# Performance work log

Measured on AMD Instinct MI355X. Metric: run time of the kernel, lower is better.

The kernel has to match this reference:

```python
import jax, jax.numpy as jnp
import numpy as np

VOCAB, EMBED, PROJ = 200000, 300, 128
B, S = 16, 2048


def setup_inputs() -> dict:
    key = jax.random.key(0)
    k1, k2, k3, k4, k5 = jax.random.split(key, 5)
    ext_word_ids = jax.random.randint(k1, (B, S), 0, VOCAB)
    seq_lengths = jax.random.randint(k2, (B,), 1, S + 1)  # at least 1 token per sentence
    embed = jax.random.normal(k3, (VOCAB, EMBED), dtype=jnp.float32)
    embed = embed.at[0].set(0.0)  # padding_idx = 0 row is zero
    W = jax.random.normal(k4, (PROJ, EMBED), dtype=jnp.float32) * 0.05
    b = jax.random.normal(k5, (PROJ,), dtype=jnp.float32) * 0.05
    return {"ext_word_ids": ext_word_ids, "seq_lengths": seq_lengths,
            "embed": embed, "W": W, "b": b}


def reference(ext_word_ids, seq_lengths, embed, W, b):
    # Dedup in the original is purely an optimization; math is:
    # out[b, t] = W @ embed[ids[b, t]] + b  for t < seq_lengths[b], else 0.
    x = embed[ext_word_ids]                       # [B, S, E] gather
    y = jnp.einsum('bse,pe->bsp', x, W) + b       # [B, S, P] projection
    mask = jnp.arange(y.shape[1])[None, :] < seq_lengths[:, None]  # [B, S]
    return jnp.where(mask[:, :, None], y, jnp.zeros((), y.dtype))
```

## Files before the change

kernel.cpp:

```cpp
#include <hip/hip_runtime.h>


#define E 300
#define P 128
#define S 2048
#define BS 32768
#define TM 64

typedef short bf16x8 __attribute__((ext_vector_type(8)));
typedef short bf16x4 __attribute__((ext_vector_type(4)));
typedef float f32x4 __attribute__((ext_vector_type(4)));

__device__ inline unsigned short f32_bf16_fast(float f) {
    unsigned int u = __builtin_bit_cast(unsigned int, f);
    return (unsigned short)((u + 0x8000u) >> 16);
}
__device__ inline bf16x8 cvt8(f32x4 a, f32x4 b) {
    bf16x8 r;
    r[0] = (short)f32_bf16_fast(a[0]); r[1] = (short)f32_bf16_fast(a[1]);
    r[2] = (short)f32_bf16_fast(a[2]); r[3] = (short)f32_bf16_fast(a[3]);
    r[4] = (short)f32_bf16_fast(b[0]); r[5] = (short)f32_bf16_fast(b[1]);
    r[6] = (short)f32_bf16_fast(b[2]); r[7] = (short)f32_bf16_fast(b[3]);
    return r;
}
__device__ inline bf16x4 cvt4(f32x4 a) {
    bf16x4 r;
    r[0] = (short)f32_bf16_fast(a[0]); r[1] = (short)f32_bf16_fast(a[1]);
    r[2] = (short)f32_bf16_fast(a[2]); r[3] = (short)f32_bf16_fast(a[3]);
    return r;
}

__global__ __launch_bounds__(256) void ft_main(
    const int* __restrict__ ids, const int* __restrict__ seqlen,
    const float* __restrict__ embed, const float* __restrict__ Wf,
    const float* __restrict__ bias, float* __restrict__ out)
{
    __shared__ unsigned char Wl[40960];

    const int tid  = threadIdx.x;
    const int wave = tid >> 6, lane = tid & 63;
    const int fr   = lane & 15, kg = lane >> 4;

    const int tile = blockIdx.x >> 1;
    const int ch   = blockIdx.x & 1;
    const int tok0 = tile * TM;
    const int bi0  = tok0 >> 11;
    const int t0   = tok0 & (S - 1);
    const int sl0  = seqlen[bi0];

    if (sl0 <= t0) {
        #pragma unroll
        for (int i = 0; i < 4; ++i) {
            int idx   = tid + i * 256;
            int token = tok0 + (idx >> 4);
            int c     = ch * 64 + (idx & 15) * 4;
            *(f32x4*)(out + (long long)token * P + c) = (f32x4){0.f, 0.f, 0.f, 0.f};
        }
        return;
    }

    const int token_a = tok0 + wave * 16 + fr;
    const long long id = ids[token_a];
    const float* __restrict__ rp = embed + id * (long long)E;

    bf16x8 av[10];
    #pragma unroll
    for (int s = 0; s < 9; ++s) {
        const int kb = s * 32 + kg * 8;
        f32x4 f0 = *(const f32x4*)(rp + kb);
        f32x4 f1 = *(const f32x4*)(rp + kb + 4);
        av[s] = cvt8(f0, f1);
    }
    {
        f32x4 z4 = {0.f, 0.f, 0.f, 0.f};
        f32x4 f0 = z4, f1 = z4;
        if (kg == 0)      { f0 = *(const f32x4*)(rp + 288); f1 = *(const f32x4*)(rp + 292); }
        else if (kg == 1) { f0 = *(const f32x4*)(rp + 296); }
        av[9] = cvt8(f0, f1);
    }

    const int R0 = ch * 64;
    #pragma unroll
    for (int i = 0; i < 20; ++i) {
        int g4 = tid + i * 256;
        int r  = g4 / 80;
        int c4 = g4 - r * 80;
        int c0 = c4 * 4;
        f32x4 v = {0.f, 0.f, 0.f, 0.f};
        if (c0 < 300)
            v = *(const f32x4*)(Wf + (long long)(R0 + r) * E + c0);
        int s   = c0 >> 5;
        int kgg = (c0 & 31) >> 3;
        int h   = (c0 >> 2) & 1;
        int ni  = r >> 4;
        int fr2 = r & 15;
        int off = (((s * 4 + ni) * 16 + fr2) << 6) + (kgg << 4) + (h << 3);
        *(bf16x4*)(Wl + off) = cvt4(v);
    }
    __syncthreads();

    f32x4 acc[4];
    #pragma unroll
    for (int ni = 0; ni < 4; ++ni) acc[ni] = (f32x4){0.f, 0.f, 0.f, 0.f};

    #pragma unroll
    for (int s = 0; s < 10; ++s) {
        #pragma unroll
        for (int ni = 0; ni < 4; ++ni) {
            bf16x8 bv = *(const bf16x8*)(Wl + ((((s * 4 + ni) * 16 + fr) << 6) + (kg << 4)));
            acc[ni] = __builtin_amdgcn_mfma_f32_16x16x32_bf16(av[s], bv, acc[ni], 0, 0, 0);
        }
    }

    float bs[4];
    #pragma unroll
    for (int ni = 0; ni < 4; ++ni) bs[ni] = bias[ch * 64 + ni * 16 + fr];

    #pragma unroll
    for (int j = 0; j < 4; ++j) {
        int orow  = wave * 16 + kg * 4 + j;
        int token = tok0 + orow;
        int t     = token & (S - 1);
        bool valid = (t < sl0);
        #pragma unroll
        for (int ni = 0; ni < 4; ++ni) {
            float v = valid ? (acc[ni][j] + bs[ni]) : 0.0f;
            out[(long long)token * P + ch * 64 + ni * 16 + fr] = v;
        }
    }
}

extern "C" void kernel_launch(void* const* d_in, const int* in_sizes, int n_in,
                              void* d_out, int out_size, void* d_ws, size_t ws_size,
                              hipStream_t stream) {
    const int*   ids    = (const int*)d_in[0];
    const int*   sl     = (const int*)d_in[1];
    const float* embed  = (const float*)d_in[2];
    const float* W      = (const float*)d_in[3];
    const float* bias   = (const float*)d_in[4];
    float*       out    = (float*)d_out;

    ft_main<<<(BS / TM) * 2, 256, 0, stream>>>(ids, sl, embed, W, bias, out);
}
```

Measured before the change: 22.73 us.

## Compute all 128 output columns per block to avoid duplicate embedding gathers

```diff
diff --git a/kernel.cpp b/kernel.cpp
--- a/kernel.cpp
+++ b/kernel.cpp
@@ -6,6 +6,7 @@
 #define S 2048
 #define BS 32768
 #define TM 64
+#define TAIL_OFF 73728
 
 typedef short bf16x8 __attribute__((ext_vector_type(8)));
 typedef short bf16x4 __attribute__((ext_vector_type(4)));
@@ -30,32 +31,28 @@
     return r;
 }
 
-__global__ __launch_bounds__(256) void ft_main(
+__global__ __launch_bounds__(256, 2) void ft_main(
     const int* __restrict__ ids, const int* __restrict__ seqlen,
     const float* __restrict__ embed, const float* __restrict__ Wf,
     const float* __restrict__ bias, float* __restrict__ out)
 {
-    __shared__ unsigned char Wl[40960];
+    __shared__ unsigned char Wl[77824];
 
     const int tid  = threadIdx.x;
     const int wave = tid >> 6, lane = tid & 63;
     const int fr   = lane & 15, kg = lane >> 4;
 
-    const int tile = blockIdx.x >> 1;
-    const int ch   = blockIdx.x & 1;
-    const int tok0 = tile * TM;
+    const int tok0 = blockIdx.x * TM;
     const int bi0  = tok0 >> 11;
     const int t0   = tok0 & (S - 1);
     const int sl0  = seqlen[bi0];
 
     if (sl0 <= t0) {
+        f32x4* o = (f32x4*)(out + (long long)tok0 * P);
+        f32x4 z = {0.f, 0.f, 0.f, 0.f};
         #pragma unroll
-        for (int i = 0; i < 4; ++i) {
-            int idx   = tid + i * 256;
-            int token = tok0 + (idx >> 4);
-            int c     = ch * 64 + (idx & 15) * 4;
-            *(f32x4*)(out + (long long)token * P + c) = (f32x4){0.f, 0.f, 0.f, 0.f};
-        }
+        for (int i = 0; i < 8; ++i)
+            o[tid + i * 256] = z;
         return;
     }
 
@@ -79,42 +76,56 @@
         av[9] = cvt8(f0, f1);
     }
 
-    const int R0 = ch * 64;
-    #pragma unroll
-    for (int i = 0; i < 20; ++i) {
+    #pragma unroll 8
+    for (int i = 0; i < 40; ++i) {
         int g4 = tid + i * 256;
         int r  = g4 / 80;
         int c4 = g4 - r * 80;
         int c0 = c4 * 4;
+        if (c0 >= 304) continue;
         f32x4 v = {0.f, 0.f, 0.f, 0.f};
         if (c0 < 300)
-            v = *(const f32x4*)(Wf + (long long)(R0 + r) * E + c0);
-        int s   = c0 >> 5;
-        int kgg = (c0 & 31) >> 3;
-        int h   = (c0 >> 2) & 1;
+            v = *(const f32x4*)(Wf + (long long)r * E + c0);
         int ni  = r >> 4;
         int fr2 = r & 15;
-        int off = (((s * 4 + ni) * 16 + fr2) << 6) + (kgg << 4) + (h << 3);
+        int off;
+        if (c0 < 288) {
+            int s   = c0 >> 5;
+            int kgg = (c0 & 31) >> 3;
+            int h   = (c0 >> 2) & 1;
+            off = (((s * 8 + ni) * 16 + fr2) << 6) + (kgg << 4) + (h << 3);
+        } else {
+            int kgm = (c0 - 288) >> 3;
+            int h   = ((c0 - 288) >> 2) & 1;
+            off = TAIL_OFF + (((ni * 16 + fr2) << 5) + (kgm << 4) + (h << 3));
+        }
         *(bf16x4*)(Wl + off) = cvt4(v);
     }
     __syncthreads();
 
-    f32x4 acc[4];
+    f32x4 acc[8];
     #pragma unroll
-    for (int ni = 0; ni < 4; ++ni) acc[ni] = (f32x4){0.f, 0.f, 0.f, 0.f};
+    for (int ni = 0; ni < 8; ++ni) acc[ni] = (f32x4){0.f, 0.f, 0.f, 0.f};
 
     #pragma unroll
-    for (int s = 0; s < 10; ++s) {
+    for (int s = 0; s < 9; ++s) {
         #pragma unroll
-        for (int ni = 0; ni < 4; ++ni) {
-            bf16x8 bv = *(const bf16x8*)(Wl + ((((s * 4 + ni) * 16 + fr) << 6) + (kg << 4)));
+        for (int ni = 0; ni < 8; ++ni) {
+            bf16x8 bv = *(const bf16x8*)(Wl + ((((s * 8 + ni) * 16 + fr) << 6) + (kg << 4)));
             acc[ni] = __builtin_amdgcn_mfma_f32_16x16x32_bf16(av[s], bv, acc[ni], 0, 0, 0);
         }
     }
+    {
+        #pragma unroll
+        for (int ni = 0; ni < 8; ++ni) {
+            bf16x8 bv = *(const bf16x8*)(Wl + TAIL_OFF + (((ni * 16 + fr) << 5) + ((kg & 1) << 4)));
+            acc[ni] = __builtin_amdgcn_mfma_f32_16x16x32_bf16(av[9], bv, acc[ni], 0, 0, 0);
+        }
+    }
 
-    float bs[4];
+    float bs[8];
     #pragma unroll
-    for (int ni = 0; ni < 4; ++ni) bs[ni] = bias[ch * 64 + ni * 16 + fr];
+    for (int ni = 0; ni < 8; ++ni) bs[ni] = bias[ni * 16 + fr];
 
     #pragma unroll
     for (int j = 0; j < 4; ++j) {
@@ -123,9 +134,9 @@
         int t     = token & (S - 1);
         bool valid = (t < sl0);
         #pragma unroll
-        for (int ni = 0; ni < 4; ++ni) {
+        for (int ni = 0; ni < 8; ++ni) {
             float v = valid ? (acc[ni][j] + bs[ni]) : 0.0f;
-            out[(long long)token * P + ch * 64 + ni * 16 + fr] = v;
+            out[(long long)token * P + ni * 16 + fr] = v;
         }
     }
 }
@@ -140,5 +151,5 @@
     const float* bias   = (const float*)d_in[4];
     float*       out    = (float*)d_out;
 
-    ft_main<<<(BS / TM) * 2, 256, 0, stream>>>(ids, sl, embed, W, bias, out);
+    ft_main<<<BS / TM, 256, 0, stream>>>(ids, sl, embed, W, bias, out);
 }
```

New measurement: 26.26 us. +15.5%, slower.

## Split gather into separate bf16 workspace pass before GEMM kernel

Applied to the files above, without the earlier changes.

```diff
diff --git a/kernel.cpp b/kernel.cpp
--- a/kernel.cpp
+++ b/kernel.cpp
@@ -6,6 +6,8 @@
 #define S 2048
 #define BS 32768
 #define TM 64
+#define WSR 304
+#define WS_NEED ((size_t)BS * WSR * 2)
 
 typedef short bf16x8 __attribute__((ext_vector_type(8)));
 typedef short bf16x4 __attribute__((ext_vector_type(4)));
@@ -30,10 +32,41 @@
     return r;
 }
 
-__global__ __launch_bounds__(256) void ft_main(
+__global__ __launch_bounds__(256) void ft_gather(
     const int* __restrict__ ids, const int* __restrict__ seqlen,
-    const float* __restrict__ embed, const float* __restrict__ Wf,
-    const float* __restrict__ bias, float* __restrict__ out)
+    const float* __restrict__ embed, unsigned short* __restrict__ ws)
+{
+    const int tid  = threadIdx.x;
+    const int tok0 = blockIdx.x * TM;
+    const int bi0  = tok0 >> 11;
+    const int t0   = tok0 & (S - 1);
+    const int sl0  = seqlen[bi0];
+    if (sl0 <= t0) return;
+
+    __shared__ int sid[TM];
+    if (tid < TM) sid[tid] = ids[tok0 + tid];
+    __syncthreads();
+
+    #pragma unroll
+    for (int i = 0; i < 19; ++i) {
+        int flat = tid + i * 256;
+        if (flat < 4800) {
+            int r  = flat / 75;
+            int c4 = flat - r * 75;
+            int token = tok0 + r;
+            int t = token & (S - 1);
+            if (t < sl0) {
+                f32x4 v = *(const f32x4*)(embed + (long long)sid[r] * E + c4 * 4);
+                *(bf16x4*)(ws + (long long)token * WSR + c4 * 4) = cvt4(v);
+            }
+        }
+    }
+}
+
+__global__ __launch_bounds__(256) void ft_gemm(
+    const int* __restrict__ seqlen, const unsigned short* __restrict__ ws,
+    const float* __restrict__ Wf, const float* __restrict__ bias,
+    float* __restrict__ out)
 {
     __shared__ unsigned char Wl[40960];
 
@@ -60,24 +93,13 @@
     }
 
     const int token_a = tok0 + wave * 16 + fr;
-    const long long id = ids[token_a];
-    const float* __restrict__ rp = embed + id * (long long)E;
+    const unsigned short* __restrict__ rp = ws + (long long)token_a * WSR;
 
     bf16x8 av[10];
     #pragma unroll
-    for (int s = 0; s < 9; ++s) {
-        const int kb = s * 32 + kg * 8;
-        f32x4 f0 = *(const f32x4*)(rp + kb);
-        f32x4 f1 = *(const f32x4*)(rp + kb + 4);
-        av[s] = cvt8(f0, f1);
-    }
-    {
-        f32x4 z4 = {0.f, 0.f, 0.f, 0.f};
-        f32x4 f0 = z4, f1 = z4;
-        if (kg == 0)      { f0 = *(const f32x4*)(rp + 288); f1 = *(const f32x4*)(rp + 292); }
-        else if (kg == 1) { f0 = *(const f32x4*)(rp + 296); }
-        av[9] = cvt8(f0, f1);
-    }
+    for (int s = 0; s < 9; ++s)
+        av[s] = *(const bf16x8*)(rp + s * 32 + kg * 8);
+    av[9] = *(const bf16x8*)(rp + 288 + (kg & 1) * 8);
 
     const int R0 = ch * 64;
     #pragma unroll
@@ -130,6 +152,102 @@
     }
 }
 
+__global__ __launch_bounds__(256) void ft_mono(
+    const int* __restrict__ ids, const int* __restrict__ seqlen,
+    const float* __restrict__ embed, const float* __restrict__ Wf,
+    const float* __restrict__ bias, float* __restrict__ out)
+{
+    __shared__ unsigned char Wl[40960];
+    const int tid  = threadIdx.x;
+    const int wave = tid >> 6, lane = tid & 63;
+    const int fr   = lane & 15, kg = lane >> 4;
+    const int tile = blockIdx.x >> 1;
+    const int ch   = blockIdx.x & 1;
+    const int tok0 = tile * TM;
+    const int bi0  = tok0 >> 11;
+    const int t0   = tok0 & (S - 1);
+    const int sl0  = seqlen[bi0];
+
+    if (sl0 <= t0) {
+        #pragma unroll
+        for (int i = 0; i < 4; ++i) {
+            int idx   = tid + i * 256;
+            int token = tok0 + (idx >> 4);
+            int c     = ch * 64 + (idx & 15) * 4;
+            *(f32x4*)(out + (long long)token * P + c) = (f32x4){0.f, 0.f, 0.f, 0.f};
+        }
+        return;
+    }
+
+    const int token_a = tok0 + wave * 16 + fr;
+    const long long id = ids[token_a];
+    const float* __restrict__ rp = embed + id * (long long)E;
+
+    bf16x8 av[10];
+    #pragma unroll
+    for (int s = 0; s < 9; ++s) {
+        const int kb = s * 32 + kg * 8;
+        f32x4 f0 = *(const f32x4*)(rp + kb);
+        f32x4 f1 = *(const f32x4*)(rp + kb + 4);
+        av[s] = cvt8(f0, f1);
+    }
+    {
+        f32x4 z4 = {0.f, 0.f, 0.f, 0.f};
+        f32x4 f0 = z4, f1 = z4;
+        if (kg == 0)      { f0 = *(const f32x4*)(rp + 288); f1 = *(const f32x4*)(rp + 292); }
+        else if (kg == 1) { f0 = *(const f32x4*)(rp + 296); }
+        av[9] = cvt8(f0, f1);
+    }
+
+    const int R0 = ch * 64;
+    #pragma unroll
+    for (int i = 0; i < 20; ++i) {
+        int g4 = tid + i * 256;
+        int r  = g4 / 80;
+        int c4 = g4 - r * 80;
+        int c0 = c4 * 4;
+        f32x4 v = {0.f, 0.f, 0.f, 0.f};
+        if (c0 < 300)
+            v = *(const f32x4*)(Wf + (long long)(R0 + r) * E + c0);
+        int s   = c0 >> 5;
+        int kgg = (c0 & 31) >> 3;
+        int h   = (c0 >> 2) & 1;
+        int ni  = r >> 4;
+        int fr2 = r & 15;
+        int off = (((s * 4 + ni) * 16 + fr2) << 6) + (kgg << 4) + (h << 3);
+        *(bf16x4*)(Wl + off) = cvt4(v);
+    }
+    __syncthreads();
+
+    f32x4 acc[4];
+    #pragma unroll
+    for (int ni = 0; ni < 4; ++ni) acc[ni] = (f32x4){0.f, 0.f, 0.f, 0.f};
+    #pragma unroll
+    for (int s = 0; s < 10; ++s) {
+        #pragma unroll
+        for (int ni = 0; ni < 4; ++ni) {
+            bf16x8 bv = *(const bf16x8*)(Wl + ((((s * 4 + ni) * 16 + fr) << 6) + (kg << 4)));
+            acc[ni] = __builtin_amdgcn_mfma_f32_16x16x32_bf16(av[s], bv, acc[ni], 0, 0, 0);
+        }
+    }
+
+    float bs[4];
+    #pragma unroll
+    for (int ni = 0; ni < 4; ++ni) bs[ni] = bias[ch * 64 + ni * 16 + fr];
+    #pragma unroll
+    for (int j = 0; j < 4; ++j) {
+        int orow  = wave * 16 + kg * 4 + j;
+        int token = tok0 + orow;
+        int t     = token & (S - 1);
+        bool valid = (t < sl0);
+        #pragma unroll
+        for (int ni = 0; ni < 4; ++ni) {
+            float v = valid ? (acc[ni][j] + bs[ni]) : 0.0f;
+            out[(long long)token * P + ch * 64 + ni * 16 + fr] = v;
+        }
+    }
+}
+
 extern "C" void kernel_launch(void* const* d_in, const int* in_sizes, int n_in,
                               void* d_out, int out_size, void* d_ws, size_t ws_size,
                               hipStream_t stream) {
@@ -140,5 +258,11 @@
     const float* bias   = (const float*)d_in[4];
     float*       out    = (float*)d_out;
 
-    ft_main<<<(BS / TM) * 2, 256, 0, stream>>>(ids, sl, embed, W, bias, out);
-}
+    if (ws_size >= WS_NEED) {
+        unsigned short* ws = (unsigned short*)d_ws;
+        ft_gather<<<BS / TM, 256, 0, stream>>>(ids, sl, embed, ws);
+        ft_gemm<<<(BS / TM) * 2, 256, 0, stream>>>(sl, ws, W, bias, out);
+    } else {
+        ft_mono<<<(BS / TM) * 2, 256, 0, stream>>>(ids, sl, embed, W, bias, out);
+    }
+}
```

After: 29.86 us. 1.31x slower.

## Process all output columns per block with smaller token tiles and two W passes

Applied to the files above, without the earlier changes.

```diff
diff --git a/kernel.cpp b/kernel.cpp
--- a/kernel.cpp
+++ b/kernel.cpp
@@ -5,7 +5,7 @@
 #define P 128
 #define S 2048
 #define BS 32768
-#define TM 64
+#define TM 32
 
 typedef short bf16x8 __attribute__((ext_vector_type(8)));
 typedef short bf16x4 __attribute__((ext_vector_type(4)));
@@ -30,7 +30,7 @@
     return r;
 }
 
-__global__ __launch_bounds__(256) void ft_main(
+__global__ __launch_bounds__(256, 4) void ft_main(
     const int* __restrict__ ids, const int* __restrict__ seqlen,
     const float* __restrict__ embed, const float* __restrict__ Wf,
     const float* __restrict__ bias, float* __restrict__ out)
@@ -40,28 +40,27 @@
     const int tid  = threadIdx.x;
     const int wave = tid >> 6, lane = tid & 63;
     const int fr   = lane & 15, kg = lane >> 4;
+    const int wm   = wave >> 1;
+    const int wn   = wave & 1;
 
-    const int tile = blockIdx.x >> 1;
-    const int ch   = blockIdx.x & 1;
-    const int tok0 = tile * TM;
+    const int tok0 = blockIdx.x * TM;
     const int bi0  = tok0 >> 11;
     const int t0   = tok0 & (S - 1);
-    const int sl0  = seqlen[bi0];
+
+    const int token_a = tok0 + wm * 16 + fr;
+    const int id = ids[token_a];
+    const int sl0 = seqlen[bi0];
 
     if (sl0 <= t0) {
+        f32x4* o = (f32x4*)(out + (long long)tok0 * P);
+        f32x4 z = {0.f, 0.f, 0.f, 0.f};
         #pragma unroll
-        for (int i = 0; i < 4; ++i) {
-            int idx   = tid + i * 256;
-            int token = tok0 + (idx >> 4);
-            int c     = ch * 64 + (idx & 15) * 4;
-            *(f32x4*)(out + (long long)token * P + c) = (f32x4){0.f, 0.f, 0.f, 0.f};
-        }
+        for (int i = 0; i < 4; ++i)
+            o[tid + i * 256] = z;
         return;
     }
 
-    const int token_a = tok0 + wave * 16 + fr;
-    const long long id = ids[token_a];
-    const float* __restrict__ rp = embed + id * (long long)E;
+    const float* __restrict__ rp = embed + (long long)id * E;
 
     bf16x8 av[10];
     #pragma unroll
@@ -79,54 +78,59 @@
         av[9] = cvt8(f0, f1);
     }
 
-    const int R0 = ch * 64;
-    #pragma unroll
-    for (int i = 0; i < 20; ++i) {
-        int g4 = tid + i * 256;
-        int r  = g4 / 80;
-        int c4 = g4 - r * 80;
-        int c0 = c4 * 4;
-        f32x4 v = {0.f, 0.f, 0.f, 0.f};
-        if (c0 < 300)
-            v = *(const f32x4*)(Wf + (long long)(R0 + r) * E + c0);
-        int s   = c0 >> 5;
-        int kgg = (c0 & 31) >> 3;
-        int h   = (c0 >> 2) & 1;
-        int ni  = r >> 4;
-        int fr2 = r & 15;
-        int off = (((s * 4 + ni) * 16 + fr2) << 6) + (kgg << 4) + (h << 3);
-        *(bf16x4*)(Wl + off) = cvt4(v);
-    }
-    __syncthreads();
+    #pragma unroll 1
+    for (int p = 0; p < 2; ++p) {
+        const int R0 = p * 64;
+        #pragma unroll 5
+        for (int i = 0; i < 20; ++i) {
+            int g4 = tid + i * 256;
+            int r  = g4 / 80;
+            int c4 = g4 - r * 80;
+            int c0 = c4 * 4;
+            f32x4 v = {0.f, 0.f, 0.f, 0.f};
+            if (c0 < 300)
+                v = *(const f32x4*)(Wf + (long long)(R0 + r) * E + c0);
+            int s   = c0 >> 5;
+            int kgg = (c0 & 31) >> 3;
+            int h   = (c0 >> 2) & 1;
+            int nq  = r >> 4;
+            int fr2 = r & 15;
+            int off = (((s * 4 + nq) * 16 + fr2) << 6) + (kgg << 4) + (h << 3);
+            *(bf16x4*)(Wl + off) = cvt4(v);
+        }
+        __syncthreads();
 
-    f32x4 acc[4];
-    #pragma unroll
-    for (int ni = 0; ni < 4; ++ni) acc[ni] = (f32x4){0.f, 0.f, 0.f, 0.f};
+        f32x4 acc[2];
+        acc[0] = (f32x4){0.f, 0.f, 0.f, 0.f};
+        acc[1] = (f32x4){0.f, 0.f, 0.f, 0.f};
 
-    #pragma unroll
-    for (int s = 0; s < 10; ++s) {
         #pragma unroll
-        for (int ni = 0; ni < 4; ++ni) {
-            bf16x8 bv = *(const bf16x8*)(Wl + ((((s * 4 + ni) * 16 + fr) << 6) + (kg << 4)));
-            acc[ni] = __builtin_amdgcn_mfma_f32_16x16x32_bf16(av[s], bv, acc[ni], 0, 0, 0);
+        for (int s = 0; s < 10; ++s) {
+            #pragma unroll
+            for (int ni = 0; ni < 2; ++ni) {
+                int nq = wn * 2 + ni;
+                bf16x8 bv = *(const bf16x8*)(Wl + ((((s * 4 + nq) * 16 + fr) << 6) + (kg << 4)));
+                acc[ni] = __builtin_amdgcn_mfma_f32_16x16x32_bf16(av[s], bv, acc[ni], 0, 0, 0);
+            }
         }
-    }
 
-    float bs[4];
-    #pragma unroll
-    for (int ni = 0; ni < 4; ++ni) bs[ni] = bias[ch * 64 + ni * 16 + fr];
+        const int cbase = p * 64 + wn * 32;
+        float bs0 = bias[cbase + fr];
+        float bs1 = bias[cbase + 16 + fr];
 
-    #pragma unroll
-    for (int j = 0; j < 4; ++j) {
-        int orow  = wave * 16 + kg * 4 + j;
-        int token = tok0 + orow;
-        int t     = token & (S - 1);
-        bool valid = (t < sl0);
         #pragma unroll
-        for (int ni = 0; ni < 4; ++ni) {
-            float v = valid ? (acc[ni][j] + bs[ni]) : 0.0f;
-            out[(long long)token * P + ch * 64 + ni * 16 + fr] = v;
+        for (int j = 0; j < 4; ++j) {
+            int orow  = wm * 16 + kg * 4 + j;
+            int token = tok0 + orow;
+            int t     = token & (S - 1);
+            bool valid = (t < sl0);
+            float v0 = valid ? (acc[0][j] + bs0) : 0.0f;
+            float v1 = valid ? (acc[1][j] + bs1) : 0.0f;
+            out[(long long)token * P + cbase + fr]      = v0;
+            out[(long long)token * P + cbase + 16 + fr] = v1;
         }
+
+        if (p == 0) __syncthreads();
     }
 }
 
@@ -140,5 +144,5 @@
     const float* bias   = (const float*)d_in[4];
     float*       out    = (float*)d_out;
 
-    ft_main<<<(BS / TM) * 2, 256, 0, stream>>>(ids, sl, embed, W, bias, out);
+    ft_main<<<BS / TM, 256, 0, stream>>>(ids, sl, embed, W, bias, out);
 }
```

Result: slower. 24.32 us (+7.0%).
